# Kernel optimization log

Measured on AMD Instinct MI355X. Metric: run time of the kernel, lower is better.

The kernel has to match this reference:

```python
import jax, jax.numpy as jnp
import numpy as np

B, D_IN, D_HID, D_OUT, E = 8192, 1024, 4096, 1024, 8


def setup_inputs() -> dict:
    key = jax.random.key(0)
    ks = jax.random.split(key, 7)
    s_in = 1.0 / np.sqrt(D_IN)
    s_hid = 1.0 / np.sqrt(D_HID)
    return {
        "x": jax.random.normal(ks[0], (B, D_IN), dtype=jnp.float32),
        "W1": jax.random.uniform(ks[1], (E, D_IN, D_HID), jnp.float32, -s_in, s_in),
        "b1": jax.random.uniform(ks[2], (E, D_HID), jnp.float32, -s_in, s_in),
        "W2": jax.random.uniform(ks[3], (E, D_HID, D_OUT), jnp.float32, -s_hid, s_hid),
        "b2": jax.random.uniform(ks[4], (E, D_OUT), jnp.float32, -s_hid, s_hid),
        "Wg": jax.random.uniform(ks[5], (D_IN, E), jnp.float32, -s_in, s_in),
        "bg": jax.random.uniform(ks[6], (E,), jnp.float32, -s_in, s_in),
    }


def reference(x, W1, b1, W2, b2, Wg, bg):
    # Gating network: softmax over experts
    gate = jax.nn.softmax(x @ Wg + bg, axis=1)                  # [B, E]
    # All-experts 2-layer MLP as batched GEMMs
    h = jax.nn.relu(jnp.einsum('bi,eih->beh', x, W1) + b1)       # [B, E, H]
    expert_out = jnp.einsum('beh,eho->beo', h, W2) + b2          # [B, E, O]
    # Gate-weighted sum over experts
    return jnp.einsum('be,beo->bo', gate, expert_out)            # [B, O]
```

## Files before the change

kernel.cpp:

```cpp
#include <hip/hip_runtime.h>
#include <hip/hip_bf16.h>
#include <stdint.h>

#define B_TOK 8192
#define DD_IN 1024
#define D_HID 4096
#define D_OUT 1024
#define N_EXP 8
#define NT    (N_EXP * D_HID)
#define SPLITK 4
#define KS    (NT / SPLITK)

typedef __attribute__((ext_vector_type(8))) __bf16 bf16x8;
typedef __attribute__((ext_vector_type(4))) float f32x4;

__global__ void gate_cvt_kernel(const float* __restrict__ x,
                                const float* __restrict__ Wg,
                                const float* __restrict__ bg,
                                float* __restrict__ gate,
                                __bf16* __restrict__ xb) {
    int wave = threadIdx.x >> 6;
    int lane = threadIdx.x & 63;
    int row  = blockIdx.x * 4 + wave;
    if (row >= B_TOK) return;
    const float* xr = x + (size_t)row * DD_IN;
    __bf16* xbr = xb + (size_t)row * DD_IN;
    float acc[N_EXP];
#pragma unroll
    for (int e = 0; e < N_EXP; ++e) acc[e] = 0.f;
#pragma unroll
    for (int c = 0; c < 4; ++c) {
        int k = (c * 64 + lane) * 4;
        float4 v = *(const float4*)&xr[k];
        __bf16 b0 = (__bf16)v.x, b1 = (__bf16)v.y, b2 = (__bf16)v.z, b3 = (__bf16)v.w;
        ushort4 u;
        u.x = *(unsigned short*)&b0; u.y = *(unsigned short*)&b1;
        u.z = *(unsigned short*)&b2; u.w = *(unsigned short*)&b3;
        *(ushort4*)&xbr[k] = u;
        const float* wg0 = Wg + (size_t)k * N_EXP;
#pragma unroll
        for (int e = 0; e < N_EXP; ++e)
            acc[e] += v.x * wg0[e] + v.y * wg0[N_EXP + e] +
                      v.z * wg0[2 * N_EXP + e] + v.w * wg0[3 * N_EXP + e];
    }
#pragma unroll
    for (int e = 0; e < N_EXP; ++e) {
        float v = acc[e];
        for (int off = 32; off; off >>= 1) v += __shfl_xor(v, off);
        acc[e] = v + bg[e];
    }
    float m = acc[0];
#pragma unroll
    for (int e = 1; e < N_EXP; ++e) m = fmaxf(m, acc[e]);
    float s = 0.f;
#pragma unroll
    for (int e = 0; e < N_EXP; ++e) { acc[e] = expf(acc[e] - m); s += acc[e]; }
    float inv = 1.f / s;
    if (lane < N_EXP) gate[(size_t)row * N_EXP + lane] = acc[lane] * inv;
}

__global__ __launch_bounds__(256)
void transpose_cvt64(const float* __restrict__ in,
                     __bf16* __restrict__ out, int R, int C,
                     long ldo, long eStride) {
    __shared__ __bf16 tile[64 * 66];
    const float* inp = in + (size_t)blockIdx.z * R * C;
    __bf16* outp = out + (size_t)blockIdx.z * eStride;
    const int c0 = blockIdx.x * 64, r0 = blockIdx.y * 64;
    const int t = threadIdx.x;
    const int lr = t >> 4;
    const int lc = (t & 15) * 4;
#pragma unroll
    for (int p = 0; p < 4; ++p) {
        int r = p * 16 + lr;
        float4 v = *(const float4*)&inp[(size_t)(r0 + r) * C + c0 + lc];
        ushort2 u01, u23;
        __bf16 b0 = (__bf16)v.x, b1 = (__bf16)v.y, b2 = (__bf16)v.z, b3 = (__bf16)v.w;
        u01.x = *(unsigned short*)&b0; u01.y = *(unsigned short*)&b1;
        u23.x = *(unsigned short*)&b2; u23.y = *(unsigned short*)&b3;
        *(ushort2*)&tile[r * 66 + lc]     = u01;
        *(ushort2*)&tile[r * 66 + lc + 2] = u23;
    }
    __syncthreads();
#pragma unroll
    for (int p = 0; p < 2; ++p) {
        int item = p * 256 + t;
        int cc = item >> 3;
        int rb = (item & 7) * 8;
        bf16x8 v;
#pragma unroll
        for (int k = 0; k < 8; ++k) v[k] = tile[(rb + k) * 66 + cc];
        *(bf16x8*)&outp[(size_t)(c0 + cc) * ldo + r0 + rb] = v;
    }
}

__device__ __forceinline__ void stage_half(const __bf16* __restrict__ gsrc, long ld,
                                           __bf16* ldsbase, int hf, long k0, int t) {
#pragma unroll
    for (int i = 0; i < 2; ++i) {
        int g = i * 512 + t;
        int rl = g >> 3, sl = g & 7;
        int r = hf * 128 + rl;
        const __bf16* src = gsrc + (size_t)r * ld + k0 + ((sl ^ (r & 7)) << 3);
        __builtin_amdgcn_global_load_lds(
            (const __attribute__((address_space(1))) void*)src,
            (__attribute__((address_space(3))) void*)(ldsbase + hf * 8192 + g * 8),
            16, 0, 0);
    }
}

__device__ __forceinline__ bf16x8 ldfrag(const __bf16* buf, int rbase, int l, int ks) {
    int r = rbase + (l & 15);
    int k = ks * 32 + ((l >> 4) << 3);
    return *(const bf16x8*)(buf + r * 64 + (k ^ ((r & 7) << 3)));
}

#define WAIT_LGKM do { asm volatile("s_waitcnt lgkmcnt(0)" ::: "memory"); \
    __builtin_amdgcn_sched_barrier(0); } while (0)
#define BAR __builtin_amdgcn_s_barrier()

#define RD_A(bufp, mb) do { \
    _Pragma("unroll") for (int mm = 0; mm < 4; ++mm) \
    _Pragma("unroll") for (int ks = 0; ks < 2; ++ks) \
        af[mm * 2 + ks] = ldfrag((bufp), wr * 128 + ((mb) + mm) * 16, l, ks); \
} while (0)
#define RD_B01(bufp) do { \
    _Pragma("unroll") for (int nn = 0; nn < 2; ++nn) \
    _Pragma("unroll") for (int ks = 0; ks < 2; ++ks) \
        bq[nn * 2 + ks] = ldfrag((bufp), wc * 64 + nn * 16, l, ks); \
} while (0)
#define RD_B23(bufp) do { \
    _Pragma("unroll") for (int nn = 2; nn < 4; ++nn) \
    _Pragma("unroll") for (int ks = 0; ks < 2; ++ks) \
        bq[nn * 2 + ks] = ldfrag((bufp), wc * 64 + nn * 16, l, ks); \
} while (0)
#define QMFMA(mb, nb) do { \
    __builtin_amdgcn_s_setprio(1); \
    _Pragma("unroll") for (int mm = 0; mm < 4; ++mm) \
    _Pragma("unroll") for (int nn = 0; nn < 2; ++nn) \
    _Pragma("unroll") for (int ks = 0; ks < 2; ++ks) \
        acc[(mb) + mm][(nb) + nn] = __builtin_amdgcn_mfma_f32_16x16x32_bf16( \
            af[mm * 2 + ks], bq[((nb) + nn) * 2 + ks], acc[(mb) + mm][(nb) + nn], 0, 0, 0); \
    __builtin_amdgcn_s_setprio(0); \
} while (0)

template <int EPI>
__global__ __launch_bounds__(512, 2)
void gemm8p(const __bf16* __restrict__ A, long lda,
            const __bf16* __restrict__ Bt, long ldb,
            int nkt, const float* __restrict__ bias,
            const float* __restrict__ gate,
            __bf16* __restrict__ outH, float* __restrict__ outP,
            long zstride) {
    __shared__ __bf16 lds[65536];
    const int t = threadIdx.x;
    const int w = t >> 6, l = t & 63;
    const int wr = w >> 2, wc = w & 3;

    const int nwg = gridDim.x * gridDim.y;
    const int orig = blockIdx.y * gridDim.x + blockIdx.x;
    const int q = nwg >> 3, r8 = nwg & 7;
    const int xcd = orig & 7, idx = orig >> 3;
    const int wg = (xcd < r8 ? xcd * (q + 1) : r8 * (q + 1) + (xcd - r8) * q) + idx;
    const long bcol = (long)(wg / gridDim.y) * 256;
    const long brow = (long)(wg % gridDim.y) * 256;
    const long kbase = (EPI == 1) ? (long)blockIdx.z * KS : 0;

    const __bf16* Atile = A + brow * lda + kbase;
    const __bf16* Btile = Bt + bcol * ldb + kbase;
    __bf16* A0 = lds;
    __bf16* A1 = lds + 16384;
    __bf16* B0 = lds + 32768;
    __bf16* B1 = lds + 49152;

    f32x4 acc[8][4];
#pragma unroll
    for (int m = 0; m < 8; ++m)
#pragma unroll
        for (int n = 0; n < 4; ++n) acc[m][n] = (f32x4)0.f;

    stage_half(Atile, lda, A0, 0, 0, t);
    stage_half(Atile, lda, A0, 1, 0, t);
    stage_half(Btile, ldb, B0, 0, 0, t);
    stage_half(Btile, ldb, B0, 1, 0, t);
    stage_half(Btile, ldb, B1, 0, 64, t);
    stage_half(Btile, ldb, B1, 1, 64, t);

    bf16x8 af[8], bq[8];
    const int niter = nkt >> 1;
    for (int it = 0; it < niter; ++it) {
        const long kb = (long)it * 128;
        const bool nl = (it < niter - 1);
        stage_half(Atile, lda, A1, 0, kb + 64, t);
        asm volatile("s_waitcnt vmcnt(6)" ::: "memory");
        __builtin_amdgcn_sched_barrier(0);
        BAR;
        RD_A(A0, 0);
        RD_B01(B0);
        WAIT_LGKM;
        QMFMA(0, 0);
        BAR;
        RD_B23(B0);
        stage_half(Atile, lda, A1, 1, kb + 64, t);
        BAR;
        WAIT_LGKM;
        QMFMA(0, 2);
        BAR;
        RD_A(A0, 4);
        if (nl) stage_half(Btile, ldb, B0, 0, kb + 128, t);
        BAR;
        WAIT_LGKM;
        QMFMA(4, 0);
        BAR;
        if (nl) stage_half(Btile, ldb, B0, 1, kb + 128, t);
        BAR;
        QMFMA(4, 2);
        BAR;
        if (nl) {
            stage_half(Atile, lda, A0, 0, kb + 128, t);
            asm volatile("s_waitcnt vmcnt(6)" ::: "memory");
        } else {
            asm volatile("s_waitcnt vmcnt(0)" ::: "memory");
        }
        __builtin_amdgcn_sched_barrier(0);
        BAR;
        RD_A(A1, 0);
        RD_B01(B1);
        WAIT_LGKM;
        QMFMA(0, 0);
        BAR;
        RD_B23(B1);
        if (nl) stage_half(Atile, lda, A0, 1, kb + 128, t);
        BAR;
        WAIT_LGKM;
        QMFMA(0, 2);
        BAR;
        RD_A(A1, 4);
        if (nl) stage_half(Btile, ldb, B1, 0, kb + 192, t);
        BAR;
        WAIT_LGKM;
        QMFMA(4, 0);
        BAR;
        if (nl) stage_half(Btile, ldb, B1, 1, kb + 192, t);
        BAR;
        QMFMA(4, 2);
        BAR;
    }

    const int ccol = (int)bcol + wc * 64 + (l & 15);
    const long crow0 = brow + wr * 128 + ((l >> 4) << 2);
    if (EPI == 0) {
        const int e = (int)(bcol >> 12);
        float bv[4];
#pragma unroll
        for (int n = 0; n < 4; ++n) bv[n] = bias[ccol + n * 16];
#pragma unroll
        for (int m = 0; m < 8; ++m)
#pragma unroll
            for (int j = 0; j < 4; ++j) {
                long row = crow0 + m * 16 + j;
                float g = gate[row * N_EXP + e];
                size_t base = (size_t)row * NT + ccol;
#pragma unroll
                for (int n = 0; n < 4; ++n)
                    outH[base + n * 16] =
                        (__bf16)(g * fmaxf(acc[m][n][j] + bv[n], 0.f));
            }
    } else {
        float* op = outP + (size_t)blockIdx.z * zstride;
#pragma unroll
        for (int m = 0; m < 8; ++m)
#pragma unroll
            for (int j = 0; j < 4; ++j) {
                long row = crow0 + m * 16 + j;
                size_t base = (size_t)row * D_OUT + ccol;
#pragma unroll
                for (int n = 0; n < 4; ++n)
                    op[base + n * 16] = acc[m][n][j];
            }
    }
}

__global__ void reduce_kernel(const float* __restrict__ partial,
                              const float* __restrict__ gate,
                              const float* __restrict__ b2,
                              float* __restrict__ out, int rows) {
    int idx = blockIdx.x * 256 + threadIdx.x;
    if (idx >= rows * 256) return;
    int r = idx >> 8;
    int c = (idx & 255) * 4;
    size_t zstride = (size_t)rows * D_OUT;
    f32x4 s = (f32x4)0.f;
#pragma unroll
    for (int ks = 0; ks < SPLITK; ++ks)
        s += *(const f32x4*)&partial[ks * zstride + (size_t)r * D_OUT + c];
#pragma unroll
    for (int e = 0; e < N_EXP; ++e) {
        float g = gate[(size_t)r * N_EXP + e];
        f32x4 bv = *(const f32x4*)&b2[(size_t)e * D_OUT + c];
        s += g * bv;
    }
    *(f32x4*)&out[(size_t)r * D_OUT + c] = s;
}

extern "C" void kernel_launch(void* const* d_in, const int* in_sizes, int n_in,
                              void* d_out, int out_size, void* d_ws, size_t ws_size,
                              hipStream_t stream) {
    const float* x  = (const float*)d_in[0];
    const float* W1 = (const float*)d_in[1];
    const float* b1 = (const float*)d_in[2];
    const float* W2 = (const float*)d_in[3];
    const float* b2 = (const float*)d_in[4];
    const float* Wg = (const float*)d_in[5];
    const float* bg = (const float*)d_in[6];
    float* out = (float*)d_out;

    char* ws = (char*)d_ws;
    size_t off = 0;
    auto take = [&](size_t bytes) {
        char* p = ws + off;
        off = (off + bytes + 255) & ~(size_t)255;
        return p;
    };
    float*  gate = (float*)take((size_t)B_TOK * N_EXP * 4);
    __bf16* xb   = (__bf16*)take((size_t)B_TOK * DD_IN * 2);
    __bf16* W1t  = (__bf16*)take((size_t)NT * DD_IN * 2);
    __bf16* W2tt = (__bf16*)take((size_t)D_OUT * NT * 2);
    size_t remain = (ws_size > off) ? (ws_size - off) : 0;
    size_t per_row = (size_t)NT * 2 + (size_t)SPLITK * D_OUT * 4;
    long Rc = (long)(remain / per_row);
    Rc &= ~255L;
    if (Rc > 4096) Rc = 4096;
    if (Rc < 256) Rc = 256;
    __bf16* h       = (__bf16*)take((size_t)Rc * NT * 2);
    float*  partial = (float*)(ws + off);

    gate_cvt_kernel<<<dim3(B_TOK / 4), dim3(256), 0, stream>>>(x, Wg, bg, gate, xb);

    transpose_cvt64<<<dim3(D_HID / 64, DD_IN / 64, N_EXP), dim3(256), 0, stream>>>(
        W1, W1t, DD_IN, D_HID, DD_IN, (long)D_HID * DD_IN);
    transpose_cvt64<<<dim3(D_OUT / 64, D_HID / 64, N_EXP), dim3(256), 0, stream>>>(
        W2, W2tt, D_HID, D_OUT, NT, D_HID);

    for (long r0 = 0; r0 < B_TOK; r0 += Rc) {
        long rows = B_TOK - r0;
        if (rows > Rc) rows = Rc;
        gemm8p<0><<<dim3(NT / 256, rows / 256), dim3(512), 0, stream>>>(
            xb + (size_t)r0 * DD_IN, DD_IN, W1t, DD_IN, DD_IN / 64,
            b1, gate + (size_t)r0 * N_EXP, h, nullptr, 0);
        gemm8p<1><<<dim3(D_OUT / 256, rows / 256, SPLITK), dim3(512), 0, stream>>>(
            h, NT, W2tt, NT, KS / 64,
            nullptr, nullptr, nullptr, partial, (long)rows * D_OUT);
        reduce_kernel<<<dim3((int)rows, 1, 1), dim3(256), 0, stream>>>(
            partial, gate + (size_t)r0 * N_EXP, b2, out + (size_t)r0 * D_OUT,
            (int)rows);
    }
}
```

Before: 1.158 ms.

## Make first GEMM persistent over eight column tiles with continuous prefetch

The first GEMM kernel now has each workgroup loop over eight consecutive 256-column output tiles for the same 256-row A block. The K-loop software pipeline runs straight across tile boundaries, so loads for the next tile are prefetched while the current tile finishes. The epilogue is written out after each tile. This removes pipeline prologue and drain per tile and lets the block reuse the A rows through cache, but it cuts the grid by 8x, which could hurt occupancy and load balance across CUs.

Result: slower. 1.310 ms (+13.1%).

```diff
diff --git a/kernel.cpp b/kernel.cpp
--- a/kernel.cpp
+++ b/kernel.cpp
@@ -118,6 +118,10 @@
 #define WAIT_LGKM do { asm volatile("s_waitcnt lgkmcnt(0)" ::: "memory"); \
     __builtin_amdgcn_sched_barrier(0); } while (0)
 #define BAR __builtin_amdgcn_s_barrier()
+#define VMC6 do { asm volatile("s_waitcnt vmcnt(6)" ::: "memory"); \
+    __builtin_amdgcn_sched_barrier(0); } while (0)
+#define VMC0 do { asm volatile("s_waitcnt vmcnt(0)" ::: "memory"); \
+    __builtin_amdgcn_sched_barrier(0); } while (0)
 
 #define RD_A(bufp, mb) do { \
     _Pragma("unroll") for (int mm = 0; mm < 4; ++mm) \
@@ -144,14 +148,135 @@
     __builtin_amdgcn_s_setprio(0); \
 } while (0)
 
-template <int EPI>
 __global__ __launch_bounds__(512, 2)
-void gemm8p(const __bf16* __restrict__ A, long lda,
+void gemm1p(const __bf16* __restrict__ A, long lda,
             const __bf16* __restrict__ Bt, long ldb,
-            int nkt, const float* __restrict__ bias,
-            const float* __restrict__ gate,
-            __bf16* __restrict__ outH, float* __restrict__ outP,
-            long zstride) {
+            const float* __restrict__ bias, const float* __restrict__ gate,
+            __bf16* __restrict__ outH) {
+    __shared__ __bf16 lds[65536];
+    const int t = threadIdx.x;
+    const int w = t >> 6, l = t & 63;
+    const int wr = w >> 2, wc = w & 3;
+
+    const int nwg = gridDim.x * gridDim.y;
+    const int orig = blockIdx.y * gridDim.x + blockIdx.x;
+    const int q = nwg >> 3, r8 = nwg & 7;
+    const int xcd = orig & 7, idx = orig >> 3;
+    const int wg = (xcd < r8 ? xcd * (q + 1) : r8 * (q + 1) + (xcd - r8) * q) + idx;
+    const int group = wg / gridDim.y;
+    const long brow = (long)(wg % gridDim.y) * 256;
+
+    const __bf16* Atile = A + brow * lda;
+    __bf16* A0 = lds;
+    __bf16* A1 = lds + 16384;
+    __bf16* B0 = lds + 32768;
+    __bf16* B1 = lds + 49152;
+
+#define SA1(ss, bufp, hf) do { if ((ss) < 128) \
+    stage_half(Atile, lda, bufp, hf, (long)((ss) & 15) << 6, t); } while (0)
+#define SB1(ss, bufp, hf) do { if ((ss) < 128) \
+    stage_half(Bt + ((size_t)(group * 8 + ((ss) >> 4))) * 256 * ldb, ldb, \
+               bufp, hf, (long)((ss) & 15) << 6, t); } while (0)
+
+    f32x4 acc[8][4];
+#pragma unroll
+    for (int m = 0; m < 8; ++m)
+#pragma unroll
+        for (int n = 0; n < 4; ++n) acc[m][n] = (f32x4)0.f;
+
+    SA1(0, A0, 0); SA1(0, A0, 1);
+    SB1(0, B0, 0); SB1(0, B0, 1);
+    SB1(1, B1, 0); SB1(1, B1, 1);
+
+    bf16x8 af[8], bq[8];
+    for (int tile = 0; tile < 8; ++tile) {
+        for (int itl = 0; itl < 8; ++itl) {
+            const int it = (tile << 3) | itl;
+            const int s0 = it << 1;
+            const bool lastg = (it == 63);
+            SA1(s0 + 1, A1, 0);
+            VMC6;
+            BAR;
+            RD_A(A0, 0);
+            RD_B01(B0);
+            WAIT_LGKM;
+            QMFMA(0, 0);
+            BAR;
+            RD_B23(B0);
+            SA1(s0 + 1, A1, 1);
+            BAR;
+            WAIT_LGKM;
+            QMFMA(0, 2);
+            BAR;
+            RD_A(A0, 4);
+            SB1(s0 + 2, B0, 0);
+            BAR;
+            WAIT_LGKM;
+            QMFMA(4, 0);
+            BAR;
+            SB1(s0 + 2, B0, 1);
+            BAR;
+            QMFMA(4, 2);
+            BAR;
+            SA1(s0 + 2, A0, 0);
+            if (lastg) { VMC0; } else { VMC6; }
+            BAR;
+            RD_A(A1, 0);
+            RD_B01(B1);
+            WAIT_LGKM;
+            QMFMA(0, 0);
+            BAR;
+            RD_B23(B1);
+            SA1(s0 + 2, A0, 1);
+            BAR;
+            WAIT_LGKM;
+            QMFMA(0, 2);
+            BAR;
+            RD_A(A1, 4);
+            SB1(s0 + 3, B1, 0);
+            BAR;
+            WAIT_LGKM;
+            QMFMA(4, 0);
+            BAR;
+            SB1(s0 + 3, B1, 1);
+            BAR;
+            QMFMA(4, 2);
+            BAR;
+        }
+        {
+            const long bcol = ((long)group * 8 + tile) * 256;
+            const int ccol = (int)bcol + wc * 64 + (l & 15);
+            const long crow0 = brow + wr * 128 + ((l >> 4) << 2);
+            const int e = group >> 1;
+            float bv[4];
+#pragma unroll
+            for (int n = 0; n < 4; ++n) bv[n] = bias[ccol + n * 16];
+#pragma unroll
+            for (int m = 0; m < 8; ++m)
+#pragma unroll
+                for (int j = 0; j < 4; ++j) {
+                    long row = crow0 + m * 16 + j;
+                    float g = gate[row * N_EXP + e];
+                    size_t base = (size_t)row * NT + ccol;
+#pragma unroll
+                    for (int n = 0; n < 4; ++n)
+                        outH[base + n * 16] =
+                            (__bf16)(g * fmaxf(acc[m][n][j] + bv[n], 0.f));
+                }
+#pragma unroll
+            for (int m = 0; m < 8; ++m)
+#pragma unroll
+                for (int n = 0; n < 4; ++n) acc[m][n] = (f32x4)0.f;
+        }
+    }
+#undef SA1
+#undef SB1
+}
+
+__global__ __launch_bounds__(512, 2)
+void gemm2_p(const __bf16* __restrict__ A, long lda,
+             const __bf16* __restrict__ Bt, long ldb,
+             int nkt, float* __restrict__ outP, long zstride) {
     __shared__ __bf16 lds[65536];
     const int t = threadIdx.x;
     const int w = t >> 6, l = t & 63;
@@ -164,7 +289,7 @@
     const int wg = (xcd < r8 ? xcd * (q + 1) : r8 * (q + 1) + (xcd - r8) * q) + idx;
     const long bcol = (long)(wg / gridDim.y) * 256;
     const long brow = (long)(wg % gridDim.y) * 256;
-    const long kbase = (EPI == 1) ? (long)blockIdx.z * KS : 0;
+    const long kbase = (long)blockIdx.z * KS;
 
     const __bf16* Atile = A + brow * lda + kbase;
     const __bf16* Btile = Bt + bcol * ldb + kbase;
@@ -192,8 +317,7 @@
         const long kb = (long)it * 128;
         const bool nl = (it < niter - 1);
         stage_half(Atile, lda, A1, 0, kb + 64, t);
-        asm volatile("s_waitcnt vmcnt(6)" ::: "memory");
-        __builtin_amdgcn_sched_barrier(0);
+        VMC6;
         BAR;
         RD_A(A0, 0);
         RD_B01(B0);
@@ -218,11 +342,10 @@
         BAR;
         if (nl) {
             stage_half(Atile, lda, A0, 0, kb + 128, t);
-            asm volatile("s_waitcnt vmcnt(6)" ::: "memory");
+            VMC6;
         } else {
-            asm volatile("s_waitcnt vmcnt(0)" ::: "memory");
+            VMC0;
         }
-        __builtin_amdgcn_sched_barrier(0);
         BAR;
         RD_A(A1, 0);
         RD_B01(B1);
@@ -249,36 +372,17 @@
 
     const int ccol = (int)bcol + wc * 64 + (l & 15);
     const long crow0 = brow + wr * 128 + ((l >> 4) << 2);
-    if (EPI == 0) {
-        const int e = (int)(bcol >> 12);
-        float bv[4];
-#pragma unroll
-        for (int n = 0; n < 4; ++n) bv[n] = bias[ccol + n * 16];
-#pragma unroll
-        for (int m = 0; m < 8; ++m)
-#pragma unroll
-            for (int j = 0; j < 4; ++j) {
-                long row = crow0 + m * 16 + j;
-                float g = gate[row * N_EXP + e];
-                size_t base = (size_t)row * NT + ccol;
-#pragma unroll
-                for (int n = 0; n < 4; ++n)
-                    outH[base + n * 16] =
-                        (__bf16)(g * fmaxf(acc[m][n][j] + bv[n], 0.f));
-            }
-    } else {
-        float* op = outP + (size_t)blockIdx.z * zstride;
-#pragma unroll
-        for (int m = 0; m < 8; ++m)
-#pragma unroll
-            for (int j = 0; j < 4; ++j) {
-                long row = crow0 + m * 16 + j;
-                size_t base = (size_t)row * D_OUT + ccol;
-#pragma unroll
-                for (int n = 0; n < 4; ++n)
-                    op[base + n * 16] = acc[m][n][j];
-            }
-    }
+    float* op = outP + (size_t)blockIdx.z * zstride;
+#pragma unroll
+    for (int m = 0; m < 8; ++m)
+#pragma unroll
+        for (int j = 0; j < 4; ++j) {
+            long row = crow0 + m * 16 + j;
+            size_t base = (size_t)row * D_OUT + ccol;
+#pragma unroll
+            for (int n = 0; n < 4; ++n)
+                op[base + n * 16] = acc[m][n][j];
+        }
 }
 
 __global__ void reduce_kernel(const float* __restrict__ partial,
@@ -345,12 +449,11 @@
     for (long r0 = 0; r0 < B_TOK; r0 += Rc) {
         long rows = B_TOK - r0;
         if (rows > Rc) rows = Rc;
-        gemm8p<0><<<dim3(NT / 256, rows / 256), dim3(512), 0, stream>>>(
-            xb + (size_t)r0 * DD_IN, DD_IN, W1t, DD_IN, DD_IN / 64,
-            b1, gate + (size_t)r0 * N_EXP, h, nullptr, 0);
-        gemm8p<1><<<dim3(D_OUT / 256, rows / 256, SPLITK), dim3(512), 0, stream>>>(
-            h, NT, W2tt, NT, KS / 64,
-            nullptr, nullptr, nullptr, partial, (long)rows * D_OUT);
+        gemm1p<<<dim3(NT / 2048, rows / 256), dim3(512), 0, stream>>>(
+            xb + (size_t)r0 * DD_IN, DD_IN, W1t, DD_IN,
+            b1, gate + (size_t)r0 * N_EXP, h);
+        gemm2_p<<<dim3(D_OUT / 256, rows / 256, SPLITK), dim3(512), 0, stream>>>(
+            h, NT, W2tt, NT, KS / 64, partial, (long)rows * D_OUT);
         reduce_kernel<<<dim3((int)rows, 1, 1), dim3(256), 0, stream>>>(
             partial, gate + (size_t)r0 * N_EXP, b2, out + (size_t)r0 * D_OUT,
             (int)rows);
```
